# Kernel optimization log

Hardware: AMD Instinct MI355X
Metric: run time of the kernel (lower is better)

The kernel has to match this reference:

```python
import jax, jax.numpy as jnp
import numpy as np

EPS = 1e-6
R_ROTS = 3
MAX_DEG = 4.0
MD = 1  # max_disp_z = max_disp_y = max_disp_x = 1
E = (2 * MD + 1) ** 3  # 27


def eul2rotm_y(ry):
    # rotation about the y axis (rx = rz = 0 in the original eul2rotm call)
    c, s = jnp.cos(ry), jnp.sin(ry)
    z, o = jnp.zeros_like(ry), jnp.ones_like(ry)
    return jnp.stack([jnp.stack([c, z, s], -1),
                      jnp.stack([z, o, z], -1),
                      jnp.stack([-s, z, c], -1)], -2)  # [N,3,3]


def merge_rt(r, t):
    N = r.shape[0]
    top = jnp.concatenate([r, t[:, :, None]], axis=2)
    bot = jnp.broadcast_to(jnp.array([[[0.0, 0.0, 0.0, 1.0]]], dtype=r.dtype), (N, 1, 4))
    return jnp.concatenate([top, bot], axis=1)  # [N,4,4]


def invert_rt(rt):
    r = rt[:, :3, :3]
    t = rt[:, :3, 3]
    rinv = jnp.swapaxes(r, 1, 2)
    tinv = -jnp.einsum('nij,nj->ni', rinv, t)
    return merge_rt(rinv, tinv)


def trilinear_sample(vox, xyz):
    # vox [N,C,Z,Y,X]; xyz [N,Z,Y,X,3] voxel-space (x,y,z) coords; zero outside
    N, C, Z, Y, X = vox.shape
    x, y, z = xyz[..., 0], xyz[..., 1], xyz[..., 2]
    x0, y0, z0 = jnp.floor(x), jnp.floor(y), jnp.floor(z)
    fx, fy, fz = x - x0, y - y0, z - z0
    voxf = vox.reshape(N, C, Z * Y * X)
    gather = jax.vmap(lambda v, i: v[:, i])  # per-batch gather over flat spatial
    out = jnp.zeros((N, C, Z, Y, X), vox.dtype)
    for dz in (0, 1):
        wz = fz if dz else (1.0 - fz)
        zc = z0 + dz
        for dy in (0, 1):
            wy = fy if dy else (1.0 - fy)
            yc = y0 + dy
            for dx in (0, 1):
                wx = fx if dx else (1.0 - fx)
                xc = x0 + dx
                valid = ((xc >= 0) & (xc <= X - 1) & (yc >= 0) & (yc <= Y - 1)
                         & (zc >= 0) & (zc <= Z - 1))
                xi = jnp.clip(xc, 0, X - 1).astype(jnp.int32)
                yi = jnp.clip(yc, 0, Y - 1).astype(jnp.int32)
                zi = jnp.clip(zc, 0, Z - 1).astype(jnp.int32)
                idx = (zi * Y + yi) * X + xi  # [N,Z,Y,X]
                vals = gather(voxf, idx.reshape(N, -1)).reshape(N, C, Z, Y, X)
                w = (wx * wy * wz * valid.astype(vox.dtype))[:, None]
                out = out + w * vals
    return out


def apply_4x4_to_vox(T, vox):
    # warp vox by rigid transform T (unit voxel size, grid-centered Mem2Ref)
    N, C, Z, Y, X = vox.shape
    Tinv = invert_rt(T)
    zz, yy, xx = jnp.meshgrid(jnp.arange(Z), jnp.arange(Y), jnp.arange(X), indexing='ij')
    grid = jnp.stack([xx, yy, zz], -1).astype(vox.dtype)  # [Z,Y,X,3] in (x,y,z)
    center = (jnp.array([X, Y, Z], vox.dtype) - 1.0) / 2.0
    ref = grid - center
    src = jnp.einsum('nij,zyxj->nzyxi', Tinv[:, :3, :3], ref) + Tinv[:, None, None, None, :3, 3]
    return trilinear_sample(vox, src + center)


def cost_volume_3d(v0, v1):
    # masked-mean correlation over C for every shift in a 3x3x3 neighborhood
    N, C, D, H, W = v0.shape
    v1p = jnp.pad(v1, ((0, 0), (0, 0), (MD, MD), (MD, MD), (MD, MD)))
    mask = jnp.pad(jnp.ones((N, 1, D, H, W), v0.dtype),
                   ((0, 0), (0, 0), (MD, MD), (MD, MD), (MD, MD)))
    costs = []
    for dz in range(2 * MD + 1):
        for dy in range(2 * MD + 1):
            for dx in range(2 * MD + 1):
                sl = v1p[:, :, dz:dz + D, dy:dy + H, dx:dx + W]
                m = mask[:, :, dz:dz + D, dy:dy + H, dx:dx + W]
                num = jnp.sum(v0 * sl, axis=1, keepdims=True)
                den = m * C  # sum of mask broadcast over C channels
                costs.append(num / (den + EPS))
    return jnp.concatenate(costs, axis=1)  # [N,27,D,H,W]


def setup_inputs() -> dict:
    key = jax.random.key(0)
    ks = jax.random.split(key, 8)
    B, C, Z, Y, X = 4, 32, 64, 32, 64
    feat0 = jax.random.normal(ks[0], (B, C, Z, Y, X), jnp.float32)
    feat1 = jax.random.normal(ks[1], (B, C, Z, Y, X), jnp.float32)
    ry_g = jax.random.uniform(ks[2], (B,), jnp.float32, -0.05, 0.05)
    t_g = 0.5 * jax.random.normal(ks[3], (B, 3), jnp.float32)
    cam0_T_cam1_g = merge_rt(eul2rotm_y(ry_g), t_g)
    fan = R_ROTS * E  # 81
    W1 = jax.random.normal(ks[4], (128, fan), jnp.float32) / np.sqrt(fan)
    b1 = jnp.zeros((128,), jnp.float32)
    W2 = jax.random.normal(ks[5], (128, 128), jnp.float32) / np.sqrt(128.0)
    b2 = jnp.zeros((128,), jnp.float32)
    W3 = jax.random.normal(ks[6], (4, 128), jnp.float32) / np.sqrt(128.0)
    b3 = jnp.zeros((4,), jnp.float32)
    return dict(feat0=feat0, feat1=feat1, cam0_T_cam1_g=cam0_T_cam1_g,
                W1=W1, b1=b1, W2=W2, b2=b2, W3=W3, b3=b3)


def reference(feat0, feat1, cam0_T_cam1_g, W1, b1, W2, b2, W3, b3):
    B, C, Z, Y, X = feat0.shape
    # candidate y-rotations, replicated per batch element
    rots = jnp.linspace(-MAX_DEG, MAX_DEG, R_ROTS)
    ry = jnp.tile(rots[None, :], (B, 1)).reshape(B * R_ROTS)
    camN_T_cam1 = merge_rt(eul2rotm_y(jnp.deg2rad(ry)), jnp.zeros((B * R_ROTS, 3), feat0.dtype))
    feat0r = jnp.repeat(feat0[:, None], R_ROTS, axis=1).reshape(B * R_ROTS, C, Z, Y, X)
    feat1r = jnp.repeat(feat1[:, None], R_ROTS, axis=1).reshape(B * R_ROTS, C, Z, Y, X)
    featN = apply_4x4_to_vox(camN_T_cam1, feat1r)
    cc = cost_volume_3d(feat0r, featN)                # [B*R,27,Z,Y,X]
    heat = jnp.sum(cc, axis=(2, 3, 4))                 # [B*R,27]
    f = heat.reshape(B, R_ROTS * E)
    f = jax.nn.leaky_relu(f, 0.1)
    f = f / (EPS + jnp.sqrt(jnp.sum(f * f, axis=1, keepdims=True)))
    f = jax.nn.leaky_relu(f @ W1.T + b1, 0.1)
    f = jax.nn.leaky_relu(f @ W2.T + b2, 0.1)
    f = f @ W3.T + b3                                  # [B,4]
    r_out, yv, xv, zv = f[:, 0], f[:, 1], f[:, 2], f[:, 3]
    # Mem2Ref is affine with unit voxel size -> delta == (x,y,z) directly
    delta = jnp.stack([xv, yv, zv], axis=1)
    cam0_T_cam1_e = merge_rt(eul2rotm_y(jnp.deg2rad(r_out)), -delta)
    feat1_warped = apply_4x4_to_vox(cam0_T_cam1_e, feat1)
    # eval_against_gt (coeffs folded to 1.0, sc=1.0)
    ry_of = lambda rt: jnp.arctan2(rt[:, 0, 2], rt[:, 2, 2])
    deg_e = jnp.rad2deg(ry_of(cam0_T_cam1_e))
    deg_g = jnp.rad2deg(ry_of(cam0_T_cam1_g))
    t_e = cam0_T_cam1_e[:, :3, 3]
    t_g = cam0_T_cam1_g[:, :3, 3]
    t_l2 = jnp.mean(jnp.sum((t_e - t_g) ** 2, axis=1))
    deg_l2 = jnp.mean((deg_e - deg_g) ** 2)
    total_loss = t_l2 + deg_l2
    return total_loss, cam0_T_cam1_e, feat1_warped
```

## Files before the change

### kernel.cpp

```cpp
#include <hip/hip_runtime.h>
#include <math.h>

#define NCH 32
#define CHV (64*32*64)
#define NB 4
#define NT2 512
#define INVC (1.0f/(32.0f+1e-6f))
#define D2R 0.017453292519943295f
#define R2D 57.29577951308232f

#define P1 72
#define F0B (32*P1)
#define UNITSZ (32*P1 + 24*P1)

__global__ __launch_bounds__(256) void k_heat(const float* __restrict__ feat0,
                                              const float* __restrict__ feat1,
                                              float* __restrict__ partial)
{
    __shared__ float L[2][UNITSZ];

    const int lid = (int)blockIdx.x;
    const int nid = (lid & 7) * 256 + (lid >> 3);
    const int yt  = nid & 7;
    const int zt  = (nid >> 3) & 31;
    const int chh = (nid >> 8) & 1;
    const int b   = nid >> 9;

    const int tid = (int)threadIdx.x;
    const int wv = tid >> 6;
    const int lane = tid & 63;
    const int tx = lane & 15, ty = lane >> 4;
    const int x0 = 4 * tx;
    const int z0 = 2 * zt;
    const bool ident = (wv == 1);

    const float* f0base = feat0 + ((size_t)b * NCH + chh * 16) * CHV;
    const float* f1base = feat1 + ((size_t)b * NCH + chh * 16) * CHV;

    int aB[2][4];
    float wAx[2][4], wBx[2][4], wZl[2][4];
    if (wv == 0 || wv == 2) {
        const float th = 4.0f * (float)(wv - 1) * D2R;
        const float cs = cosf(th), sn = sinf(th);
        #pragma unroll
        for (int k = 0; k < 2; ++k) {
            #pragma unroll
            for (int i = 0; i < 4; ++i) {
                const float rx = (float)(x0 + i) - 31.5f;
                const float rz = (float)(z0 + k) - 31.5f;
                const float sx = cs * rx - sn * rz + 31.5f;
                const float sz = sn * rx + cs * rz + 31.5f;
                const float xf = floorf(sx), zf = floorf(sz);
                const float fx = sx - xf, fz = sz - zf;
                const int ix = (int)xf, iz = (int)zf;
                int bx; float A_, B_;
                if (ix == -1)      { bx = 0;  A_ = fx;        B_ = 0.0f; }
                else if (ix == 63) { bx = 62; A_ = 0.0f;      B_ = 1.0f - fx; }
                else if ((unsigned)ix <= 62u) { bx = ix; A_ = 1.0f - fx; B_ = fx; }
                else               { bx = 0;  A_ = 0.0f;      B_ = 0.0f; }
                wAx[k][i] = A_; wBx[k][i] = B_;
                wZl[k][i] = 1.0f - fz;
                const int zl = min(max(iz - (2 * zt - 3), 0), 6);
                aB[k][i] = (zl * 4 + ty) * P1 + bx;
            }
        }
    }
    const int iA0 = (12 + ty) * P1 + x0;
    const int iA1 = iA0 + 4 * P1;
    const int fb0 = F0B + ty * P1 + x0;

    float acc[27];
    #pragma unroll
    for (int o = 0; o < 27; ++o) acc[o] = 0.0f;

#define STAGE_CH(CHN)                                                           \
    {                                                                           \
        const int u_ = (CHN) & 1;                                               \
        const float* f1c_ = f1base + (size_t)(CHN) * CHV;                       \
        const float* f0c_ = f0base + (size_t)(CHN) * CHV;                       \
        float* Ln_ = &L[u_][0];                                                 \
        const int tq_ = lane >> 4, c4_ = (lane & 15) << 2;                      \
        float4 v1_[8], v0_[6];                                                  \
        _Pragma("unroll")                                                       \
        for (int k_ = 0; k_ < 8; ++k_) {                                        \
            const int zs_ = 2 * zt - 3 + k_;                                    \
            v1_[k_] = (float4){0.0f, 0.0f, 0.0f, 0.0f};                         \
            if (zs_ >= 0 && zs_ < 64)                                           \
                v1_[k_] = *(const float4*)(f1c_ + zs_ * 2048                    \
                            + (4 * yt + tq_) * 64 + c4_);                       \
        }                                                                       \
        _Pragma("unroll")                                                       \
        for (int k_ = 0; k_ < 6; ++k_) {                                        \
            const int r_ = 4 * k_ + tq_;                                        \
            const int i_ = (r_ * 43) >> 8;                                      \
            const int j_ = r_ - 6 * i_;                                         \
            const int zf_ = 2 * zt - 1 + i_;                                    \
            const int yf_ = 4 * yt - 1 + j_;                                    \
            v0_[k_] = (float4){0.0f, 0.0f, 0.0f, 0.0f};                         \
            if (zf_ >= 0 && zf_ < 64 && yf_ >= 0 && yf_ < 32)                   \
                v0_[k_] = *(const float4*)(f0c_ + zf_ * 2048 + yf_ * 64 + c4_); \
        }                                                                       \
        _Pragma("unroll")                                                       \
        for (int k_ = 0; k_ < 8; ++k_)                                          \
            *(float4*)&Ln_[(4 * k_ + tq_) * P1 + c4_] = v1_[k_];                \
        _Pragma("unroll")                                                       \
        for (int k_ = 0; k_ < 6; ++k_)                                          \
            *(float4*)&Ln_[F0B + (4 * k_ + tq_) * P1 + c4_] = v0_[k_];          \
    }

#define ROWFMA(KK, OZP1, YRI, R)                                                \
    { const int base_ = (OZP1) * 9 + (2 - (YRI)) * 3;                           \
      acc[base_ + 0] += g0[KK]*R.x + fr[KK][0]*R.y + fr[KK][1]*R.z + fr[KK][2]*R.w; \
      acc[base_ + 1] += fr[KK][0]*R.x + fr[KK][1]*R.y + fr[KK][2]*R.z + fr[KK][3]*R.w; \
      acc[base_ + 2] += fr[KK][1]*R.x + fr[KK][2]*R.y + fr[KK][3]*R.z + g5[KK]*R.w; }

    if (wv == 3) STAGE_CH(0)
    __syncthreads();

    #pragma unroll 1
    for (int ch = 0; ch < 16; ++ch) {
        if (wv == 3) {
            if (ch + 1 < 16) STAGE_CH(ch + 1)
        } else {
            const float* Lb = &L[ch & 1][0];

            float fr[2][4];
            if (ident) {
                const float4 v0 = *(const float4*)&Lb[iA0];
                const float4 v1 = *(const float4*)&Lb[iA1];
                fr[0][0] = v0.x; fr[0][1] = v0.y; fr[0][2] = v0.z; fr[0][3] = v0.w;
                fr[1][0] = v1.x; fr[1][1] = v1.y; fr[1][2] = v1.z; fr[1][3] = v1.w;
            } else {
                #pragma unroll
                for (int k = 0; k < 2; ++k) {
                    #pragma unroll
                    for (int i = 0; i < 4; ++i) {
                        const int a = aB[k][i];
                        const float p00 = Lb[a], p01 = Lb[a + 1];
                        const float p10 = Lb[a + 4 * P1], p11 = Lb[a + 4 * P1 + 1];
                        const float sLo = wAx[k][i] * p00 + wBx[k][i] * p01;
                        const float sHi = wAx[k][i] * p10 + wBx[k][i] * p11;
                        fr[k][i] = sHi + wZl[k][i] * (sLo - sHi);
                    }
                }
            }

            float g0[2], g5[2];
            #pragma unroll
            for (int k = 0; k < 2; ++k) {
                const float a_ = __shfl_up(fr[k][3], 1, 64);
                const float c_ = __shfl_down(fr[k][0], 1, 64);
                g0[k] = (tx == 0) ? 0.0f : a_;
                g5[k] = (tx == 15) ? 0.0f : c_;
            }

            __builtin_amdgcn_s_setprio(1);
            #pragma unroll
            for (int zri = 0; zri < 4; ++zri) {
                const float4 R0 = *(const float4*)&Lb[fb0 + (zri * 6 + 0) * P1];
                const float4 R1 = *(const float4*)&Lb[fb0 + (zri * 6 + 1) * P1];
                const float4 R2 = *(const float4*)&Lb[fb0 + (zri * 6 + 2) * P1];
                if (zri == 0) { ROWFMA(0, 2, 0, R0) ROWFMA(0, 2, 1, R1) ROWFMA(0, 2, 2, R2) }
                if (zri == 1) { ROWFMA(0, 1, 0, R0) ROWFMA(0, 1, 1, R1) ROWFMA(0, 1, 2, R2)
                                ROWFMA(1, 2, 0, R0) ROWFMA(1, 2, 1, R1) ROWFMA(1, 2, 2, R2) }
                if (zri == 2) { ROWFMA(0, 0, 0, R0) ROWFMA(0, 0, 1, R1) ROWFMA(0, 0, 2, R2)
                                ROWFMA(1, 1, 0, R0) ROWFMA(1, 1, 1, R1) ROWFMA(1, 1, 2, R2) }
                if (zri == 3) { ROWFMA(1, 0, 0, R0) ROWFMA(1, 0, 1, R1) ROWFMA(1, 0, 2, R2) }
            }
            __builtin_amdgcn_s_setprio(0);
        }
        __syncthreads();
    }
#undef ROWFMA
#undef STAGE_CH

    if (wv < 3) {
        const int slot = (zt * 8 + yt) * 2 + chh;
        #pragma unroll 1
        for (int o = 0; o < 27; ++o) {
            float v = acc[o];
            #pragma unroll
            for (int d = 32; d >= 1; d >>= 1) v += __shfl_down(v, d, 64);
            if (lane == 0)
                partial[((size_t)((b * 3 + wv) * 27) + o) * NT2 + slot] = v;
        }
    }
}

__global__ __launch_bounds__(256) void k_mlp(const float* __restrict__ partial,
                                             const float* __restrict__ camg,
                                             const float* __restrict__ W1,
                                             const float* __restrict__ b1,
                                             const float* __restrict__ W2,
                                             const float* __restrict__ b2,
                                             const float* __restrict__ W3,
                                             const float* __restrict__ b3,
                                             float* __restrict__ out,
                                             float* __restrict__ params)
{
    __shared__ float heat[324];
    __shared__ float f[81];
    __shared__ float h1[128];
    __shared__ float h2[128];
    __shared__ float denom_s;
    __shared__ float res[NB][8];
    const int tid = (int)threadIdx.x;

    for (int r = tid; r < 324; r += 256) {
        const float4* p = (const float4*)(partial + (size_t)r * NT2);
        float s0 = 0.0f, s1 = 0.0f, s2 = 0.0f, s3 = 0.0f;
        #pragma unroll 4
        for (int i = 0; i < NT2 / 4; ++i) {
            const float4 v = p[i];
            s0 += v.x; s1 += v.y; s2 += v.z; s3 += v.w;
        }
        heat[r] = ((s0 + s1) + (s2 + s3)) * INVC;
    }
    __syncthreads();

    for (int b = 0; b < NB; ++b) {
        if (tid < 81) {
            float v = heat[b * 81 + tid];
            f[tid] = (v >= 0.0f) ? v : 0.1f * v;
        }
        __syncthreads();
        if (tid == 0) {
            float ss = 0.0f;
            for (int k = 0; k < 81; ++k) ss += f[k] * f[k];
            denom_s = 1e-6f + sqrtf(ss);
        }
        __syncthreads();
        if (tid < 81) f[tid] = f[tid] / denom_s;
        __syncthreads();
        if (tid < 128) {
            float a = b1[tid];
            const float* wr = W1 + tid * 81;
            for (int k = 0; k < 81; ++k) a += wr[k] * f[k];
            h1[tid] = (a >= 0.0f) ? a : 0.1f * a;
        }
        __syncthreads();
        if (tid < 128) {
            float a = b2[tid];
            const float* wr = W2 + tid * 128;
            for (int k = 0; k < 128; ++k) a += wr[k] * h1[k];
            h2[tid] = (a >= 0.0f) ? a : 0.1f * a;
        }
        __syncthreads();
        if (tid < 4) {
            float a = b3[tid];
            const float* wr = W3 + tid * 128;
            for (int k = 0; k < 128; ++k) a += wr[k] * h2[k];
            res[b][4 + tid] = a;
        }
        __syncthreads();
        if (tid == 0) {
            const float r_out = res[b][4], yv = res[b][5], xv = res[b][6], zv = res[b][7];
            const float t2 = r_out * D2R;
            const float c2 = cosf(t2), s2 = sinf(t2);
            float* m = out + 1 + b * 16;
            m[0] = c2;  m[1] = 0.0f; m[2] = s2;  m[3] = -xv;
            m[4] = 0.0f; m[5] = 1.0f; m[6] = 0.0f; m[7] = -yv;
            m[8] = -s2; m[9] = 0.0f; m[10] = c2; m[11] = -zv;
            m[12] = 0.0f; m[13] = 0.0f; m[14] = 0.0f; m[15] = 1.0f;
            params[b * 8 + 0] = c2;
            params[b * 8 + 1] = s2;
            params[b * 8 + 2] = c2 * xv - s2 * zv;
            params[b * 8 + 3] = yv;
            params[b * 8 + 4] = s2 * xv + c2 * zv;
            res[b][0] = -xv; res[b][1] = -yv; res[b][2] = -zv;
            res[b][3] = atan2f(s2, c2) * R2D;
        }
        __syncthreads();
    }

    if (tid == 0) {
        float tl2 = 0.0f, dl2 = 0.0f;
        for (int b = 0; b < NB; ++b) {
            const float* g = camg + b * 16;
            const float dx = res[b][0] - g[3];
            const float dy = res[b][1] - g[7];
            const float dz = res[b][2] - g[11];
            tl2 += dx * dx + dy * dy + dz * dz;
            const float dg = atan2f(g[2], g[10]) * R2D;
            const float dd = res[b][3] - dg;
            dl2 += dd * dd;
        }
        out[0] = tl2 * 0.25f + dl2 * 0.25f;
    }
}

__global__ __launch_bounds__(256) void k_warp(const float* __restrict__ feat1,
                                              const float* __restrict__ params,
                                              float* __restrict__ outw)
{
    const int b = blockIdx.y;
    const int p = (int)blockIdx.x * 256 + (int)threadIdx.x;
    const int z = p >> 11;
    const int y = (p >> 6) & 31;
    const int x = p & 63;

    const float cs = params[b * 8 + 0], sn = params[b * 8 + 1];
    const float tpx = params[b * 8 + 2], tpy = params[b * 8 + 3], tpz = params[b * 8 + 4];

    const float rx = (float)x - 31.5f;
    const float ry = (float)y - 15.5f;
    const float rz = (float)z - 31.5f;
    const float sx = cs * rx - sn * rz + tpx + 31.5f;
    const float sy = ry + tpy + 15.5f;
    const float sz = sn * rx + cs * rz + tpz + 31.5f;

    const float xf = floorf(sx), yf = floorf(sy), zf = floorf(sz);
    const float fx = sx - xf, fy = sy - yf, fz = sz - zf;
    const int ix = (int)xf, iy = (int)yf, iz = (int)zf;

    const float wx[2] = {1.0f - fx, fx};
    const float wy[2] = {1.0f - fy, fy};
    const float wz[2] = {1.0f - fz, fz};
    const int xs[2] = {min(max(ix, 0), 63), min(max(ix + 1, 0), 63)};
    const int ys[2] = {min(max(iy, 0), 31), min(max(iy + 1, 0), 31)};
    const int zs[2] = {min(max(iz, 0), 63), min(max(iz + 1, 0), 63)};
    const bool vx[2] = {(unsigned)ix < 64u, (unsigned)(ix + 1) < 64u};
    const bool vy[2] = {(unsigned)iy < 32u, (unsigned)(iy + 1) < 32u};
    const bool vz[2] = {(unsigned)iz < 64u, (unsigned)(iz + 1) < 64u};

    int idx[8]; float w[8];
    int q = 0;
    #pragma unroll
    for (int dz = 0; dz < 2; ++dz)
        #pragma unroll
        for (int dy = 0; dy < 2; ++dy)
            #pragma unroll
            for (int dx = 0; dx < 2; ++dx) {
                idx[q] = zs[dz] * 2048 + ys[dy] * 64 + xs[dx];
                w[q] = (vx[dx] && vy[dy] && vz[dz]) ? wx[dx] * wy[dy] * wz[dz] : 0.0f;
                ++q;
            }

    const float* f1b = feat1 + (size_t)b * NCH * CHV;
    float* ob = outw + (size_t)b * NCH * CHV;
    #pragma unroll 1
    for (int c = 0; c < NCH; ++c) {
        const float* f1c = f1b + (size_t)c * CHV;
        float a = 0.0f;
        #pragma unroll
        for (int k = 0; k < 8; ++k) a += w[k] * f1c[idx[k]];
        ob[(size_t)c * CHV + p] = a;
    }
}

extern "C" void kernel_launch(void* const* d_in, const int* in_sizes, int n_in,
                              void* d_out, int out_size, void* d_ws, size_t ws_size,
                              hipStream_t stream)
{
    (void)in_sizes; (void)n_in; (void)out_size; (void)ws_size;
    const float* feat0 = (const float*)d_in[0];
    const float* feat1 = (const float*)d_in[1];
    const float* camg  = (const float*)d_in[2];
    const float* W1 = (const float*)d_in[3];
    const float* b1 = (const float*)d_in[4];
    const float* W2 = (const float*)d_in[5];
    const float* b2 = (const float*)d_in[6];
    const float* W3 = (const float*)d_in[7];
    const float* b3 = (const float*)d_in[8];
    float* out = (float*)d_out;

    float* partial = (float*)d_ws;
    float* params  = partial + 324 * NT2;

    hipLaunchKernelGGL(k_heat, dim3(2048), dim3(256), 0, stream,
                       feat0, feat1, partial);
    hipLaunchKernelGGL(k_mlp, dim3(1), dim3(256), 0, stream,
                       partial, camg, W1, b1, W2, b2, W3, b3, out, params);
    dim3 g3((64*32*64) / 256, NB);
    hipLaunchKernelGGL(k_warp, g3, dim3(256), 0, stream, feat1, params, out + 65);
}
```

Baseline: 213.2 us.

## Split heat partial reduction into parallel kernel, shrink LDS pitch, unroll warp loop

The reduction of the 324x512 partial sums moves out of the single-block MLP kernel into a new 324-block kernel, with one block per row, wave shuffles and a final add. The MLP kernel then only loads 324 precomputed values and runs with 128 threads. The LDS row pitch in k_heat drops from 72 to 68 floats, and the channel loop in k_warp is unrolled by 2 so more gathers are in flight. The extra kernel launch adds fixed cost, and the pitch change can alter LDS bank conflicts in either direction.

Measured after the change: 215.0 us. About the same (+0.9%).

```diff
diff --git a/kernel.cpp b/kernel.cpp
--- a/kernel.cpp
+++ b/kernel.cpp
@@ -9,7 +9,7 @@
 #define D2R 0.017453292519943295f
 #define R2D 57.29577951308232f
 
-#define P1 72
+#define P1 68
 #define F0B (32*P1)
 #define UNITSZ (32*P1 + 24*P1)
 
@@ -187,7 +187,24 @@
     }
 }
 
-__global__ __launch_bounds__(256) void k_mlp(const float* __restrict__ partial,
+__global__ __launch_bounds__(128) void k_hsum(const float* __restrict__ partial,
+                                              float* __restrict__ heatw)
+{
+    __shared__ float red[2];
+    const int r = (int)blockIdx.x;
+    const int tid = (int)threadIdx.x;
+    const int lane = tid & 63, wid = tid >> 6;
+
+    const float4 v = ((const float4*)(partial + (size_t)r * NT2))[tid];
+    float s = (v.x + v.y) + (v.z + v.w);
+    #pragma unroll
+    for (int d = 32; d >= 1; d >>= 1) s += __shfl_down(s, d, 64);
+    if (lane == 0) red[wid] = s;
+    __syncthreads();
+    if (tid == 0) heatw[r] = (red[0] + red[1]) * INVC;
+}
+
+__global__ __launch_bounds__(128) void k_mlp(const float* __restrict__ heatw,
                                              const float* __restrict__ camg,
                                              const float* __restrict__ W1,
                                              const float* __restrict__ b1,
@@ -206,16 +223,7 @@
     __shared__ float res[NB][8];
     const int tid = (int)threadIdx.x;
 
-    for (int r = tid; r < 324; r += 256) {
-        const float4* p = (const float4*)(partial + (size_t)r * NT2);
-        float s0 = 0.0f, s1 = 0.0f, s2 = 0.0f, s3 = 0.0f;
-        #pragma unroll 4
-        for (int i = 0; i < NT2 / 4; ++i) {
-            const float4 v = p[i];
-            s0 += v.x; s1 += v.y; s2 += v.z; s3 += v.w;
-        }
-        heat[r] = ((s0 + s1) + (s2 + s3)) * INVC;
-    }
+    for (int p = tid; p < 324; p += 128) heat[p] = heatw[p];
     __syncthreads();
 
     for (int b = 0; b < NB; ++b) {
@@ -232,14 +240,14 @@
         __syncthreads();
         if (tid < 81) f[tid] = f[tid] / denom_s;
         __syncthreads();
-        if (tid < 128) {
+        {
             float a = b1[tid];
             const float* wr = W1 + tid * 81;
             for (int k = 0; k < 81; ++k) a += wr[k] * f[k];
             h1[tid] = (a >= 0.0f) ? a : 0.1f * a;
         }
         __syncthreads();
-        if (tid < 128) {
+        {
             float a = b2[tid];
             const float* wr = W2 + tid * 128;
             for (int k = 0; k < 128; ++k) a += wr[k] * h1[k];
@@ -338,7 +346,7 @@
 
     const float* f1b = feat1 + (size_t)b * NCH * CHV;
     float* ob = outw + (size_t)b * NCH * CHV;
-    #pragma unroll 1
+    #pragma unroll 2
     for (int c = 0; c < NCH; ++c) {
         const float* f1c = f1b + (size_t)c * CHV;
         float a = 0.0f;
@@ -366,11 +374,13 @@
 
     float* partial = (float*)d_ws;
     float* params  = partial + 324 * NT2;
+    float* heatw   = params + 32;
 
     hipLaunchKernelGGL(k_heat, dim3(2048), dim3(256), 0, stream,
                        feat0, feat1, partial);
-    hipLaunchKernelGGL(k_mlp, dim3(1), dim3(256), 0, stream,
-                       partial, camg, W1, b1, W2, b2, W3, b3, out, params);
+    hipLaunchKernelGGL(k_hsum, dim3(324), dim3(128), 0, stream, partial, heatw);
+    hipLaunchKernelGGL(k_mlp, dim3(1), dim3(128), 0, stream,
+                       heatw, camg, W1, b1, W2, b2, W3, b3, out, params);
     dim3 g3((64*32*64) / 256, NB);
     hipLaunchKernelGGL(k_warp, g3, dim3(256), 0, stream, feat1, params, out + 65);
 }
```
